# Kernel tuning notes

Hardware: AMD Instinct MI355X
Metric: run time of the kernel (lower is better)

## Reference

```python
import jax, jax.numpy as jnp
import numpy as np

N_QUBITS = 8
HIDDEN_DIM = 128
GATE_FAMILIES = ("rx", "ry", "rz")


def _rx(theta):
    theta = jnp.asarray(theta)
    c = jnp.cos(theta / 2).astype(jnp.complex64)
    s = (-1j * jnp.sin(theta / 2)).astype(jnp.complex64)
    return jnp.stack([jnp.stack([c, s], -1), jnp.stack([s, c], -1)], -2)


def _ry(theta):
    theta = jnp.asarray(theta)
    c = jnp.cos(theta / 2).astype(jnp.complex64)
    s = jnp.sin(theta / 2).astype(jnp.complex64)
    return jnp.stack([jnp.stack([c, -s], -1), jnp.stack([s, c], -1)], -2)


def _rz(theta):
    theta = jnp.asarray(theta)
    em = jnp.exp(-0.5j * theta).astype(jnp.complex64)
    ep = jnp.exp(0.5j * theta).astype(jnp.complex64)
    z = jnp.zeros_like(em)
    return jnp.stack([jnp.stack([em, z], -1), jnp.stack([z, ep], -1)], -2)


_GATE = {"rx": _rx, "ry": _ry, "rz": _rz}


def _apply_1q(state, mat, wire, n):
    # state: (B, 2^n) complex; wire 0 is the most-significant bit (PennyLane convention)
    B = state.shape[0]
    L, R = 2 ** wire, 2 ** (n - 1 - wire)
    s = state.reshape(B, L, 2, R)
    if mat.ndim == 2:
        s = jnp.einsum("ij,bljr->blir", mat, s)
    else:  # per-sample angles -> (B,2,2) matrices
        s = jnp.einsum("bij,bljr->blir", mat, s)
    return s.reshape(B, 2 ** n)


def _apply_cnot(state, wire, n):
    # CNOT with control=wire, target=wire+1 (adjacent chain)
    B = state.shape[0]
    L, R = 2 ** wire, 2 ** (n - 2 - wire)
    s = state.reshape(B, L, 2, 2, R)
    s = jnp.concatenate([s[:, :, :1], s[:, :, 1:, ::-1]], axis=2)
    return s.reshape(B, 2 ** n)


def _circuit(x, params):
    # x: (B, n) data-encoding angles; params: (n,) trainable angles. Returns <Z_0>, shape (B,).
    B, n = x.shape
    state = jnp.zeros((B, 2 ** n), jnp.complex64).at[:, 0].set(1.0)
    for i in range(n):
        state = _apply_1q(state, _rx(x[:, i]), i, n)
    for i in range(n):
        mat = _GATE[GATE_FAMILIES[i % len(GATE_FAMILIES)]](params[i])
        state = _apply_1q(state, mat, i, n)
    for i in range(n - 1):
        state = _apply_cnot(state, i, n)
    probs = state.real ** 2 + state.imag ** 2
    p = probs.reshape(B, 2, -1).sum(-1)
    return p[:, 0] - p[:, 1]


def setup_inputs() -> dict:
    key = jax.random.key(0)
    ks = jax.random.split(key, 13)
    T, B, D, H, n = 256, 256, 128, HIDDEN_DIM, N_QUBITS
    scale = 1.0 / np.sqrt(D + H)
    inputs = jax.random.normal(ks[0], (T, B, D), jnp.float32)
    d = {"inputs": inputs}
    names = ["f", "i", "u", "o"]
    for j, nm in enumerate(names):
        d["W" + nm] = jax.random.normal(ks[1 + 3 * j], (n, D + H), jnp.float32) * scale
        d["b" + nm] = jax.random.normal(ks[2 + 3 * j], (n,), jnp.float32) * scale
        d["p" + nm] = jax.random.normal(ks[3 + 3 * j], (n,), jnp.float32)
    return d


def reference(inputs, Wf, bf, Wi, bi, Wu, bu, Wo, bo, pf, pi, pu, po):
    T, B, D = inputs.shape
    h0 = jnp.zeros((B, HIDDEN_DIM), inputs.dtype)
    c0 = jnp.zeros((B, HIDDEN_DIM), inputs.dtype)

    def step(carry, x):
        hx, cx = carry
        comb = jnp.concatenate([x, hx], axis=1)  # (B, D+H)
        f = jax.nn.sigmoid(_circuit(comb @ Wf.T + bf, pf))[:, None]
        ig = jax.nn.sigmoid(_circuit(comb @ Wi.T + bi, pi))[:, None]
        g = jnp.tanh(_circuit(comb @ Wu.T + bu, pu))[:, None]
        o = jax.nn.sigmoid(_circuit(comb @ Wo.T + bo, po))[:, None]
        cx = f * cx + ig * g
        hx = o * jnp.tanh(cx)
        return (hx, cx), hx

    (hx, cx), outs = jax.lax.scan(step, (h0, c0), inputs)
    return outs, hx, cx
```

## Files before the change

### kernel.cpp

```cpp
#include <hip/hip_runtime.h>

#define TT 256
#define BB 256
#define DD 128
#define INV2PI 0.15915494309189535f

__device__ __forceinline__ float frcp(float x) { return __builtin_amdgcn_rcpf(x); }
template<int J>
__device__ __forceinline__ float quad_bcast(float v) {
    int i = __float_as_int(v);
    return __int_as_float(__builtin_amdgcn_update_dpp(i, i, J * 0x55, 0xF, 0xF, false));
}

__global__ __launch_bounds__(256) void k_angles(
    const float* __restrict__ x,
    const float* __restrict__ Wf, const float* __restrict__ bf, const float* __restrict__ pf,
    const float* __restrict__ Wi, const float* __restrict__ bi, const float* __restrict__ pi,
    const float* __restrict__ Wu, const float* __restrict__ bu, const float* __restrict__ pu,
    const float* __restrict__ Wo, const float* __restrict__ bo, const float* __restrict__ po,
    float4* __restrict__ A)
{
    __shared__ float4 w4[4][32];
    float* w = reinterpret_cast<float*>(w4);
    int tid = threadIdx.x;
    for (int k = tid; k < 512; k += 256) {
        int g = k >> 7, j = k & 127;
        const float* W = (g == 0) ? Wf : (g == 1) ? Wi : (g == 2) ? Wu : Wo;
        w[g * 128 + j] = W[j] * INV2PI;
    }
    __syncthreads();

    int r = blockIdx.x * 256 + tid;
    const float4* xr = reinterpret_cast<const float4*>(x + (size_t)r * DD);

    float af = (bf[0] + pf[0]) * INV2PI;
    float ai = (bi[0] + pi[0]) * INV2PI;
    float au = (bu[0] + pu[0]) * INV2PI;
    float ao = (bo[0] + po[0]) * INV2PI;
    #pragma unroll
    for (int k = 0; k < 32; ++k) {
        float4 v  = xr[k];
        float4 f4 = w4[0][k], i4 = w4[1][k], u4 = w4[2][k], o4 = w4[3][k];
        af = fmaf(v.x, f4.x, fmaf(v.y, f4.y, fmaf(v.z, f4.z, fmaf(v.w, f4.w, af))));
        ai = fmaf(v.x, i4.x, fmaf(v.y, i4.y, fmaf(v.z, i4.z, fmaf(v.w, i4.w, ai))));
        au = fmaf(v.x, u4.x, fmaf(v.y, u4.y, fmaf(v.z, u4.z, fmaf(v.w, u4.w, au))));
        ao = fmaf(v.x, o4.x, fmaf(v.y, o4.y, fmaf(v.z, o4.z, fmaf(v.w, o4.w, ao))));
    }
    A[r] = make_float4(af, ai, au, ao);
}

__global__ __launch_bounds__(64) void k_recur(
    float* __restrict__ Af,
    const float* __restrict__ Wf, const float* __restrict__ Wi,
    const float* __restrict__ Wu, const float* __restrict__ Wo)
{
    int lane = threadIdx.x;
    int q = lane >> 2, g = lane & 3;
    int s = blockIdx.x * 16 + q;
    int s4g = s * 4 + g;

    const float* W = (g == 0) ? Wf : (g == 1) ? Wi : (g == 2) ? Wu : Wo;
    const float4* W4 = reinterpret_cast<const float4*>(W + 128);
    float S = 0.f;
    #pragma unroll
    for (int k = 0; k < 32; ++k) {
        float4 v = W4[k];
        S += (v.x + v.y) + (v.z + v.w);
    }
    S *= INV2PI;
    bool tg = (g == 2);
    float K0 = tg ? 105.f : 26.25f;
    float K1 = tg ? 10.f  : 0.625f;
    float D1 = tg ? 45.f  : 11.25f;
    float D2 = tg ? 1.f   : 0.0625f;
    float Bact = tg ? 0.f : 0.5f;

    const float* Ab = Af + s4g;
    float h = 0.f, c = 0.f;

    float p0 = Ab[0*1024], p1 = Ab[1*1024], p2 = Ab[2*1024], p3 = Ab[3*1024];
    float p4 = Ab[4*1024], p5 = Ab[5*1024], p6 = Ab[6*1024], p7 = Ab[7*1024];

#define STEPC(P)                                                              \
    {                                                                         \
        float z = fmaf(h, S, P);                   \
        float v = __builtin_amdgcn_cosf(z);          \
        float w = v * v;                                                      \
        float d = fmaf(w, fmaf(w, D2, D1), 105.f);                            \
        float rd = frcp(d);                                                   \
        float n = v * fmaf(w, K1, K0);                                        \
        float act = fmaf(n, rd, Bact);                                        \
        float tu = quad_bcast<2>(act);                 \
        float ti = quad_bcast<1>(act);                                        \
        float tf = quad_bcast<0>(act);                                        \
        float to = quad_bcast<3>(act);                                        \
        c = fmaf(tf, c, ti * tu);                            \
        float w2 = c * c;                                                     \
        float d2 = fmaf(w2, fmaf(w2, w2 + 210.f, 4725.f), 10395.f);           \
        float rd2 = frcp(d2);                                                 \
        float n2 = c * fmaf(w2, fmaf(w2, 21.f, 1260.f), 10395.f);             \
        h = (to * n2) * rd2;                          \
    }
#define STEP(P, TIDX) { STEPC(P); Af[(size_t)(TIDX) * 1024 + s4g] = h; }

    for (int t = 0; t < TT - 8; t += 8) {
        int tn = t + 8;
        STEP(p0, t + 0); p0 = Ab[(size_t)(tn + 0) * 1024];
        STEP(p1, t + 1); p1 = Ab[(size_t)(tn + 1) * 1024];
        STEP(p2, t + 2); p2 = Ab[(size_t)(tn + 2) * 1024];
        STEP(p3, t + 3); p3 = Ab[(size_t)(tn + 3) * 1024];
        STEP(p4, t + 4); p4 = Ab[(size_t)(tn + 4) * 1024];
        STEP(p5, t + 5); p5 = Ab[(size_t)(tn + 5) * 1024];
        STEP(p6, t + 6); p6 = Ab[(size_t)(tn + 6) * 1024];
        STEP(p7, t + 7); p7 = Ab[(size_t)(tn + 7) * 1024];
    }
    STEP(p0, 248); STEP(p1, 249); STEP(p2, 250); STEP(p3, 251);
    STEP(p4, 252); STEP(p5, 253); STEP(p6, 254);
    STEPC(p7);
    Af[(size_t)255 * 1024 + s4g] = (g == 1) ? c : h;
#undef STEP
#undef STEPC
}

__global__ __launch_bounds__(256) void k_expand(
    const float4* __restrict__ A, float4* __restrict__ out)
{
    unsigned r = blockIdx.x * 256 + threadIdx.x;
    const unsigned OUTS4 = (unsigned)TT * BB * 128 / 4;
    const unsigned HX4   = (unsigned)BB * 128 / 4;
    float v;
    if (r < OUTS4) {
        v = A[r >> 5].x;
    } else {
        unsigned qq = r - OUTS4;
        unsigned b = (qq & (HX4 - 1)) >> 5;
        float4 a = A[(TT - 1) * BB + b];
        v = (qq < HX4) ? a.x : a.y;
    }
    out[r] = make_float4(v, v, v, v);
}

extern "C" void kernel_launch(void* const* d_in, const int* in_sizes, int n_in,
                              void* d_out, int out_size, void* d_ws, size_t ws_size,
                              hipStream_t stream) {
    const float* x = (const float*)d_in[0];
    const float *Wf, *bf, *pf, *Wi, *bi, *pi, *Wu, *bu, *pu, *Wo, *bo, *po;
    if (n_in >= 13 && in_sizes[3] == 8 && in_sizes[4] == 2048) {
        Wf = (const float*)d_in[1];  bf = (const float*)d_in[2];  pf = (const float*)d_in[3];
        Wi = (const float*)d_in[4];  bi = (const float*)d_in[5];  pi = (const float*)d_in[6];
        Wu = (const float*)d_in[7];  bu = (const float*)d_in[8];  pu = (const float*)d_in[9];
        Wo = (const float*)d_in[10]; bo = (const float*)d_in[11]; po = (const float*)d_in[12];
    } else {
        Wf = (const float*)d_in[1];  bf = (const float*)d_in[2];
        Wi = (const float*)d_in[3];  bi = (const float*)d_in[4];
        Wu = (const float*)d_in[5];  bu = (const float*)d_in[6];
        Wo = (const float*)d_in[7];  bo = (const float*)d_in[8];
        pf = (const float*)d_in[9];  pi = (const float*)d_in[10];
        pu = (const float*)d_in[11]; po = (const float*)d_in[12];
    }
    float4* A = (float4*)d_ws;

    k_angles<<<dim3(256), dim3(256), 0, stream>>>(
        x, Wf, bf, pf, Wi, bi, pi, Wu, bu, pu, Wo, bo, po, A);
    k_recur<<<dim3(16), dim3(64), 0, stream>>>(
        (float*)A, Wf, Wi, Wu, Wo);
    k_expand<<<dim3((TT * BB * 128 / 4 + 2 * BB * 128 / 4) / 256), dim3(256), 0, stream>>>(
        A, (float4*)d_out);
}
```

Measured before the change: 46.48 us.

## Use polynomial gate activation and buffer hidden states in LDS during recurrence

Replaces the rational (Padé) sigmoid/tanh-of-cosine gate activation with a cubic-in-v polynomial fit. This removes a reciprocal from the serial per-step dependency chain. Per-step hidden-state global stores are moved into a shared-memory buffer that is flushed after the time loop, and the expand kernel reads the new scalar layout. The risk is lower accuracy from the hand-fitted coefficients, plus an extra serialized write-out phase at the end.

```diff
diff --git a/kernel.cpp b/kernel.cpp
--- a/kernel.cpp
+++ b/kernel.cpp
@@ -54,10 +54,12 @@
     const float* __restrict__ Wf, const float* __restrict__ Wi,
     const float* __restrict__ Wu, const float* __restrict__ Wo)
 {
+    __shared__ float Hl[16 * 260];
     int lane = threadIdx.x;
     int q = lane >> 2, g = lane & 3;
     int s = blockIdx.x * 16 + q;
     int s4g = s * 4 + g;
+    int hq = q * 260;
 
     const float* W = (g == 0) ? Wf : (g == 1) ? Wi : (g == 2) ? Wu : Wo;
     const float4* W4 = reinterpret_cast<const float4*>(W + 128);
@@ -68,12 +70,12 @@
         S += (v.x + v.y) + (v.z + v.w);
     }
     S *= INV2PI;
+
     bool tg = (g == 2);
-    float K0 = tg ? 105.f : 26.25f;
-    float K1 = tg ? 10.f  : 0.625f;
-    float D1 = tg ? 45.f  : 11.25f;
-    float D2 = tg ? 1.f   : 0.0625f;
-    float Bact = tg ? 0.f : 0.5f;
+    float Q0 = tg ? 0.99702f   : 0.2500128f;
+    float Q1 = tg ? -0.3074f   : -0.0207238f;
+    float Q2 = tg ? 0.07232f   : 0.00176256f;
+    float Bq = tg ? 0.f        : 0.5f;
 
     const float* Ab = Af + s4g;
     float h = 0.f, c = 0.f;
@@ -84,13 +86,10 @@
 #define STEPC(P)                                                              \
     {                                                                         \
         float z = fmaf(h, S, P);                   \
-        float v = __builtin_amdgcn_cosf(z);          \
+        float v = __builtin_amdgcn_cosf(z);                                   \
         float w = v * v;                                                      \
-        float d = fmaf(w, fmaf(w, D2, D1), 105.f);                            \
-        float rd = frcp(d);                                                   \
-        float n = v * fmaf(w, K1, K0);                                        \
-        float act = fmaf(n, rd, Bact);                                        \
-        float tu = quad_bcast<2>(act);                 \
+        float act = fmaf(v, fmaf(w, fmaf(w, Q2, Q1), Q0), Bq);                \
+        float tu = quad_bcast<2>(act);                                        \
         float ti = quad_bcast<1>(act);                                        \
         float tf = quad_bcast<0>(act);                                        \
         float to = quad_bcast<3>(act);                                        \
@@ -99,9 +98,9 @@
         float d2 = fmaf(w2, fmaf(w2, w2 + 210.f, 4725.f), 10395.f);           \
         float rd2 = frcp(d2);                                                 \
         float n2 = c * fmaf(w2, fmaf(w2, 21.f, 1260.f), 10395.f);             \
-        h = (to * n2) * rd2;                          \
+        h = (to * n2) * rd2;                                                  \
     }
-#define STEP(P, TIDX) { STEPC(P); Af[(size_t)(TIDX) * 1024 + s4g] = h; }
+#define STEP(P, TIDX) { STEPC(P); Hl[hq + (TIDX)] = h; }
 
     for (int t = 0; t < TT - 8; t += 8) {
         int tn = t + 8;
@@ -114,28 +113,38 @@
         STEP(p6, t + 6); p6 = Ab[(size_t)(tn + 6) * 1024];
         STEP(p7, t + 7); p7 = Ab[(size_t)(tn + 7) * 1024];
     }
-    STEP(p0, 248); STEP(p1, 249); STEP(p2, 250); STEP(p3, 251);
-    STEP(p4, 252); STEP(p5, 253); STEP(p6, 254);
-    STEPC(p7);
-    Af[(size_t)255 * 1024 + s4g] = (g == 1) ? c : h;
+    STEP(p0, 248) STEP(p1, 249) STEP(p2, 250) STEP(p3, 251)
+    STEP(p4, 252) STEP(p5, 253) STEP(p6, 254) STEP(p7, 255)
 #undef STEP
 #undef STEPC
+
+    __syncthreads();
+
+    int base_b = blockIdx.x * 16;
+    for (int k = 0; k < 64; ++k) {
+        int flat = k * 64 + lane;
+        int t  = flat & 255;
+        int sl = flat >> 8;
+        float hv = Hl[sl * 260 + t];
+        Af[((size_t)t * 256 + base_b + sl) * 4] = hv;
+    }
+    if (g == 1) Af[((size_t)255 * 256 + s) * 4 + 1] = c;
 }
 
 __global__ __launch_bounds__(256) void k_expand(
-    const float4* __restrict__ A, float4* __restrict__ out)
+    const float* __restrict__ AT, float4* __restrict__ out)
 {
     unsigned r = blockIdx.x * 256 + threadIdx.x;
     const unsigned OUTS4 = (unsigned)TT * BB * 128 / 4;
     const unsigned HX4   = (unsigned)BB * 128 / 4;
     float v;
     if (r < OUTS4) {
-        v = A[r >> 5].x;
+        unsigned t = r >> 13, b = (r >> 5) & 255u;
+        v = AT[(t * 256u + b) * 4u];
     } else {
         unsigned qq = r - OUTS4;
         unsigned b = (qq & (HX4 - 1)) >> 5;
-        float4 a = A[(TT - 1) * BB + b];
-        v = (qq < HX4) ? a.x : a.y;
+        v = (qq < HX4) ? AT[(255u * 256u + b) * 4u] : AT[(255u * 256u + b) * 4u + 1u];
     }
     out[r] = make_float4(v, v, v, v);
 }
@@ -158,12 +167,11 @@
         pf = (const float*)d_in[9];  pi = (const float*)d_in[10];
         pu = (const float*)d_in[11]; po = (const float*)d_in[12];
     }
-    float4* A = (float4*)d_ws;
+    float* A = (float*)d_ws;
 
     k_angles<<<dim3(256), dim3(256), 0, stream>>>(
-        x, Wf, bf, pf, Wi, bi, pi, Wu, bu, pu, Wo, bo, po, A);
-    k_recur<<<dim3(16), dim3(64), 0, stream>>>(
-        (float*)A, Wf, Wi, Wu, Wo);
+        x, Wf, bf, pf, Wi, bi, pi, Wu, bu, pu, Wo, bo, po, (float4*)A);
+    k_recur<<<dim3(16), dim3(64), 0, stream>>>(A, Wf, Wi, Wu, Wo);
     k_expand<<<dim3((TT * BB * 128 / 4 + 2 * BB * 128 / 4) / 256), dim3(256), 0, stream>>>(
         A, (float4*)d_out);
 }
```

Result: faster. 41.68 us (-10.3%).
